# Kernel optimization log

Measured on AMD Instinct MI355X. Metric: run time of the kernel, lower is better.

The kernel has to match this reference:

```python
import jax, jax.numpy as jnp
import numpy as np

B, N, S = 64, 256, 2000
BETA = 0.95
K = int(round(S * (1.0 - BETA)))  # = 100, exact top-k CVaR reformulation
BIL = 4
SAFETY = 0.5
T_DF = 5.0
JITTER = 1e-4  # CHOLESKY_JITTER
N_ITERS = 200


def setup_inputs() -> dict:
    key = jax.random.key(0)
    k1, k2, k3 = jax.random.split(key, 3)
    mu = 0.01 * jax.random.normal(k1, (B, N), dtype=jnp.float32)
    # PSD covariance: sigma = A A^T / N
    A = 0.02 * jax.random.normal(k2, (B, N, N), dtype=jnp.float32)
    sigma = jnp.einsum('bij,bkj->bik', A, A) / N
    # standardized Student-T noise (matches _sample_noise with df>2)
    eps = jax.random.t(k3, T_DF, (B, S, N)) / jnp.sqrt(T_DF / (T_DF - 2.0))
    return {'mu': mu, 'sigma': sigma, 'eps': eps.astype(jnp.float32),
            'is_crisis': 1, 'lambda_risk': 0}


def _simplex_proj(v, z):
    # Euclidean projection of each row of v onto {x >= 0, sum(x) = z}
    n = v.shape[-1]
    u = jnp.flip(jnp.sort(v, axis=-1), axis=-1)          # descending
    css = jnp.cumsum(u, axis=-1) - z
    ind = jnp.arange(1, n + 1, dtype=v.dtype)
    rho = jnp.sum((u - css / ind) > 0, axis=-1)           # (B,) >= 1
    theta = jnp.take_along_axis(css, rho[:, None] - 1, axis=-1) / rho[:, None].astype(v.dtype)
    return jnp.maximum(v - theta, 0.0)


def _solve_cvar(R, floor):
    # minimize CVaR_beta(-R w) = mean of top-K scenario losses,
    # s.t. sum(w)=1, w>=0, w[BIL] >= floor[BIL]  (projected subgradient)
    b, n = R.shape[0], R.shape[2]
    mass = 1.0 - floor.sum()

    def proj(w):
        return _simplex_proj(w - floor, mass) + floor

    w0 = proj(jnp.full((b, n), 1.0 / n, dtype=R.dtype))

    def step(w, t):
        losses = -jnp.einsum('bsn,bn->bs', R, w)          # (B,S)
        thresh = jax.lax.top_k(losses, K)[0][:, -1:]      # K-th largest loss
        m = (losses >= thresh).astype(R.dtype)
        m = m / jnp.maximum(m.sum(-1, keepdims=True), float(K))
        g = -jnp.einsum('bs,bsn->bn', m, R)               # subgradient of top-K mean
        lr = 0.5 / jnp.sqrt(t + 1.0)
        return proj(w - lr * g), None

    w, _ = jax.lax.scan(step, w0, jnp.arange(N_ITERS, dtype=R.dtype))
    return w


def reference(mu, sigma, eps, is_crisis, lambda_risk):
    # 1) Cholesky reparameterization sampling: R = mu + eps @ L^T
    L = jnp.linalg.cholesky(sigma + JITTER * jnp.eye(N, dtype=sigma.dtype))
    R = mu[:, None, :] + jnp.einsum('bsn,bmn->bsm', eps, L)  # (B,S,N)
    if lambda_risk > 0:
        R = R + mu[:, None, :] / max(float(lambda_risk), 0.1)
    # 2) safety floor on BIL when in crisis
    floor = jnp.zeros((N,), dtype=mu.dtype).at[BIL].set(SAFETY * float(is_crisis))
    # 3) batched CVaR solve
    w = _solve_cvar(R, floor)
    # 4) post clamp + renormalize (as in the torch forward)
    w = jnp.maximum(w, 0.0)
    return w / (w.sum(-1, keepdims=True) + 1e-8)
```

## Files before the change

kernel.cpp:

```cpp
#include <hip/hip_runtime.h>
#include <stdint.h>

#define B_   64
#define N_   256
#define S_   2000
#define K_   100
#define BIL_ 4
#define NITER_ 200
#define JITTER_ 1e-4f
#define SAFETY_ 0.5f
#define PART_ 4
#define SCH_  (S_ / PART_)
#define GS_   50

#define OFF_LC16  ((size_t)0)
#define OFF_LR16  (OFF_LC16 + (size_t)B_ * N_ * N_ / 2)
#define OFF_GT    (OFF_LR16 + (size_t)B_ * N_ * N_ / 2)
#define OFF_GR    (OFF_GT + (size_t)B_ * N_ * S_ / 2)
#define OFF_LOSS  (OFF_GR + (size_t)B_ * S_ * N_ / 2)
#define OFF_BAR   (OFF_LOSS + (size_t)2 * B_ * S_)

__device__ __forceinline__ float wred_f(float x) {
#pragma unroll
  for (int off = 32; off > 0; off >>= 1) x += __shfl_xor(x, off);
  return x;
}
__device__ __forceinline__ int wred_i(int x) {
#pragma unroll
  for (int off = 32; off > 0; off >>= 1) x += __shfl_xor(x, off);
  return x;
}
__device__ __forceinline__ unsigned keyd(float x) {
  unsigned u = __float_as_uint(x);
  unsigned ku = (u & 0x80000000u) ? ~u : (u | 0x80000000u);
  return ~ku;
}
__device__ __forceinline__ uint16_t f2b(float f) {
  uint32_t u = __float_as_uint(f);
  uint32_t r = u + 0x7FFFu + ((u >> 16) & 1u);
  return (uint16_t)(r >> 16);
}
__device__ __forceinline__ float blo(uint32_t u) { return __uint_as_float(u << 16); }
__device__ __forceinline__ float bhi(uint32_t u) { return __uint_as_float(u & 0xFFFF0000u); }

__device__ __forceinline__ float michelot4(const float vp[4], float z) {
  bool act[4] = {true, true, true, true};
  float theta = 0.0f;
  int prev = -1;
  for (int pass = 0; pass < 300; ++pass) {
    float ls = 0.0f; int lc = 0;
#pragma unroll
    for (int j = 0; j < 4; ++j) { if (act[j]) { ls += vp[j]; lc += 1; } }
    ls = wred_f(ls);
    lc = wred_i(lc);
    theta = (ls - z) / (float)lc;
    if (lc == prev) break;
    prev = lc;
#pragma unroll
    for (int j = 0; j < 4; ++j) act[j] = (vp[j] > theta);
  }
  return theta;
}

__device__ __forceinline__ void proj_store(const float y[4], float fl_bil, float mass, float muf,
                                           const float* __restrict__ muB, int ln,
                                           float* w_s, float* c_sh) {
  float vp[4];
#pragma unroll
  for (int j = 0; j < 4; ++j) {
    const int n = 4 * ln + j;
    vp[j] = y[j] - ((n == BIL_) ? fl_bil : 0.0f);
  }
  const float theta = michelot4(vp, mass);
  const float4 m4 = *(const float4*)(muB + 4 * ln);
  const float mm[4] = {m4.x, m4.y, m4.z, m4.w};
  float wj[4];
  float cp = 0.0f;
#pragma unroll
  for (int j = 0; j < 4; ++j) {
    const int n = 4 * ln + j;
    wj[j] = fmaxf(vp[j] - theta, 0.0f) + ((n == BIL_) ? fl_bil : 0.0f);
    cp = fmaf(muf * mm[j], wj[j], cp);
  }
  cp = wred_f(cp);
  if (ln == 0) *c_sh = cp;
  *(float4*)(w_s + 4 * ln) = make_float4(wj[0], wj[1], wj[2], wj[3]);
}

__global__ __launch_bounds__(512) void chol_kernel(const float* __restrict__ sigma,
                                                   float* __restrict__ Lc) {
  const int b = blockIdx.x;
  const int tid = threadIdx.x;
  const int i = tid & 255;
  const int half = tid >> 8;
  const float* Sg = sigma + (size_t)b * N_ * N_;
  float* L = Lc + (size_t)b * N_ * N_;
  __shared__ __align__(16) float slab[248 * 8];
  __shared__ __align__(16) float spart[256][8];
  __shared__ __align__(16) float pnl[64];

  for (int j0 = 0; j0 < N_; j0 += 8) {
    for (int x = tid; x < j0 * 8; x += 512) {
      const int k = x >> 3, jj = x & 7;
      slab[x] = L[(size_t)k * N_ + (j0 + jj)];
    }
    float s[8];
    if (half == 0) {
#pragma unroll
      for (int jj = 0; jj < 8; ++jj) {
        float a = Sg[(size_t)(j0 + jj) * N_ + i];
        if (i == j0 + jj) a += JITTER_;
        s[jj] = a;
      }
    } else {
#pragma unroll
      for (int jj = 0; jj < 8; ++jj) s[jj] = 0.0f;
    }
    __syncthreads();

    const int kb = half ? (j0 >> 1) : 0;
    const int ke = half ? j0 : (j0 >> 1);
#pragma unroll 4
    for (int k = kb; k < ke; ++k) {
      const float lk = L[(size_t)k * N_ + i];
      const float4 h0 = *(const float4*)&slab[k * 8];
      const float4 h1 = *(const float4*)&slab[k * 8 + 4];
      s[0] = fmaf(-lk, h0.x, s[0]);
      s[1] = fmaf(-lk, h0.y, s[1]);
      s[2] = fmaf(-lk, h0.z, s[2]);
      s[3] = fmaf(-lk, h0.w, s[3]);
      s[4] = fmaf(-lk, h1.x, s[4]);
      s[5] = fmaf(-lk, h1.y, s[5]);
      s[6] = fmaf(-lk, h1.z, s[6]);
      s[7] = fmaf(-lk, h1.w, s[7]);
    }
    if (half == 1) {
      *(float4*)&spart[i][0] = make_float4(s[0], s[1], s[2], s[3]);
      *(float4*)&spart[i][4] = make_float4(s[4], s[5], s[6], s[7]);
    }
    __syncthreads();

    if (half == 0) {
      const float4 p0 = *(const float4*)&spart[i][0];
      const float4 p1 = *(const float4*)&spart[i][4];
      s[0] += p0.x; s[1] += p0.y; s[2] += p0.z; s[3] += p0.w;
      s[4] += p1.x; s[5] += p1.y; s[6] += p1.z; s[7] += p1.w;
      if ((i >> 3) == (j0 >> 3)) {
        const int base = j0 & 63;
        const int r = i & 7;
        float l[8], di[8];
#pragma unroll
        for (int m = 0; m < 8; ++m) {
          const float smv = __shfl(s[m], base + m);
          const float d = sqrtf(smv);
          const float dinv = 1.0f / d;
          di[m] = dinv;
          float lm;
          if (r == m) lm = d;
          else if (r > m) lm = s[m] * dinv;
          else lm = 0.0f;
          l[m] = lm;
#pragma unroll
          for (int mm = m + 1; mm < 8; ++mm) {
            s[mm] = fmaf(-lm, __shfl(lm, base + mm), s[mm]);
          }
        }
#pragma unroll
        for (int m = 0; m < 8; ++m) pnl[r * 8 + m] = (m < r) ? l[m] : ((m == r) ? di[r] : 0.0f);
#pragma unroll
        for (int m = 0; m < 8; ++m) L[(size_t)(j0 + m) * N_ + i] = l[m];
      }
    }
    __syncthreads();

    if (half == 0 && (i >> 3) != (j0 >> 3)) {
      float l[8];
      if (i > j0) {
#pragma unroll
        for (int m = 0; m < 8; ++m) {
          float sm = s[m];
#pragma unroll
          for (int mm = 0; mm < 8; ++mm) {
            if (mm < m) sm = fmaf(-l[mm], pnl[m * 8 + mm], sm);
          }
          l[m] = sm * pnl[m * 8 + m];
        }
      } else {
#pragma unroll
        for (int m = 0; m < 8; ++m) l[m] = 0.0f;
      }
#pragma unroll
      for (int m = 0; m < 8; ++m) L[(size_t)(j0 + m) * N_ + i] = l[m];
    }
    __syncthreads();
  }
}

__global__ __launch_bounds__(256) void lpack_kernel(const float* __restrict__ Lc,
                                                    uint16_t* __restrict__ Lr16) {
  const int b = blockIdx.x;
  const float* Lp = Lc + (size_t)b * N_ * N_;
  uint16_t* R16 = Lr16 + (size_t)b * N_ * N_;
  __shared__ float tl[32][33];
  const int tx = threadIdx.x & 31;
  const int ty = threadIdx.x >> 5;
  for (int kt = 0; kt < 8; ++kt) {
    for (int it = 0; it < 8; ++it) {
#pragma unroll
      for (int rr = 0; rr < 4; ++rr) {
        const int k = kt * 32 + ty + 8 * rr;
        const int ii = it * 32 + tx;
        tl[ty + 8 * rr][tx] = Lp[(size_t)k * N_ + ii];
      }
      __syncthreads();
#pragma unroll
      for (int rr = 0; rr < 4; ++rr) {
        const int ii = it * 32 + ty + 8 * rr;
        const int k = kt * 32 + tx;
        R16[(size_t)ii * N_ + k] = f2b(tl[tx][ty + 8 * rr]);
      }
      __syncthreads();
    }
  }
}

__global__ __launch_bounds__(256) void g_kernel(const float* __restrict__ eps,
                                                const uint16_t* __restrict__ Lr16,
                                                uint16_t* __restrict__ GT16,
                                                uint16_t* __restrict__ GR16,
                                                int* __restrict__ bar) {
  const int b = blockIdx.x;
  const int s0 = blockIdx.y * GS_;
  const int t = threadIdx.x;
  if (b == 0 && blockIdx.y == 0 && t < 64) bar[t] = 0;
  __shared__ __align__(16) uint16_t esh[GS_][N_];
  const float* E = eps + ((size_t)b * S_ + s0) * N_;
  for (int p = 0; p < GS_; ++p) esh[p][t] = f2b(E[(size_t)p * N_ + t]);
  __syncthreads();

  const uint32_t* Lrow = (const uint32_t*)(Lr16 + (size_t)b * N_ * N_) + (size_t)t * (N_ / 2);
  float acc[GS_];
#pragma unroll
  for (int s = 0; s < GS_; ++s) acc[s] = 0.0f;
  const int jmax = (t >> 1) + 1;
  for (int j = 0; j < jmax; ++j) {
    const uint32_t lu = Lrow[j];
    const float l0 = blo(lu), l1 = bhi(lu);
#pragma unroll
    for (int s = 0; s < GS_; ++s) {
      const uint32_t eu = *(const uint32_t*)&esh[s][2 * j];
      acc[s] = fmaf(l1, bhi(eu), fmaf(l0, blo(eu), acc[s]));
    }
  }
  uint16_t* GRb = GR16 + ((size_t)b * S_ + s0) * N_ + t;
  for (int s = 0; s < GS_; ++s) GRb[(size_t)s * N_] = f2b(acc[s]);
  uint32_t* GTb = (uint32_t*)(GT16 + (size_t)b * N_ * S_ + (size_t)t * S_ + s0);
#pragma unroll
  for (int u = 0; u < GS_ / 2; ++u) {
    const uint32_t pk = (uint32_t)f2b(acc[2 * u]) | ((uint32_t)f2b(acc[2 * u + 1]) << 16);
    GTb[u] = pk;
  }
}

__global__ __launch_bounds__(1024) void solve_kernel(
    const float* __restrict__ mu, const int* __restrict__ pcrisis,
    const int* __restrict__ plam, const uint16_t* __restrict__ GT16,
    const uint16_t* __restrict__ GR16, unsigned* __restrict__ lossbits,
    int* __restrict__ bar, float* __restrict__ out) {
  const int bx = blockIdx.x;
  const int b = bx & (B_ - 1);
  const int part = bx >> 6;
  const int t = threadIdx.x;
  const int ln = t & 63;
  const int s0 = part * SCH_;

  __shared__ __align__(16) float w_s[N_];
  __shared__ __align__(16) float scratch[8][N_];
  __shared__ __align__(16) uint16_t lists[S_];
  __shared__ __align__(16) int hist[4][256];
  __shared__ float c_sh;
  __shared__ int lcnt;
  __shared__ float sum_sh;

  const int crisis = pcrisis[0];
  const int lamv = plam[0];
  const float muf = 1.0f + ((lamv > 0) ? (1.0f / fmaxf((float)lamv, 0.1f)) : 0.0f);
  const float fl_bil = SAFETY_ * (float)crisis;
  const float mass = 1.0f - fl_bil;

  const float* muB = mu + (size_t)b * N_;
  const uint32_t* GTB = (const uint32_t*)(GT16 + (size_t)b * N_ * S_);
  const uint32_t* GRB = (const uint32_t*)(GR16 + (size_t)b * S_ * N_);
  float* sc1 = &scratch[0][0];

  const int q = t >> 8;
  const int idx = t & 255;
  const uint32_t* gcol = GTB + (size_t)(64 * q) * (S_ / 2) + (s0 >> 1) + idx;

  if (t < 64) {
    float y[4];
#pragma unroll
    for (int j = 0; j < 4; ++j) y[j] = 1.0f / (float)N_;
    proj_store(y, fl_bil, mass, muf, muB, ln, w_s, &c_sh);
  }
  __syncthreads();

  for (int it = 0; it < NITER_; ++it) {
    if (idx < SCH_ / 2) {
      float a0 = 0.0f, a1 = 0.0f;
#pragma unroll 8
      for (int j = 0; j < 64; ++j) {
        const uint32_t u = gcol[(size_t)j * (S_ / 2)];
        const float ww = w_s[64 * q + j];
        a0 = fmaf(blo(u), ww, a0);
        a1 = fmaf(bhi(u), ww, a1);
      }
      *(float2*)&sc1[q * SCH_ + 2 * idx] = make_float2(a0, a1);
    }
    __syncthreads();

    unsigned* lgbuf = lossbits + ((it & 1) ? (size_t)B_ * S_ : 0) + (size_t)b * S_;
    if (t < SCH_) {
      const float lv = -(c_sh + ((sc1[t] + sc1[SCH_ + t]) + (sc1[2 * SCH_ + t] + sc1[3 * SCH_ + t])));
      __hip_atomic_store(&lgbuf[s0 + t], keyd(lv), __ATOMIC_RELAXED, __HIP_MEMORY_SCOPE_AGENT);
    } else if (t >= 512) {
      for (int x = t - 512; x < 4 * 256; x += 512) ((int*)hist)[x] = 0;
      if (t == 512) lcnt = 0;
    }
    __syncthreads();

    if (t == 0) {
      __hip_atomic_fetch_add(&bar[b], 1, __ATOMIC_RELAXED, __HIP_MEMORY_SCOPE_AGENT);
      const int target = PART_ * (it + 1);
      while (__hip_atomic_load(&bar[b], __ATOMIC_RELAXED, __HIP_MEMORY_SCOPE_AGENT) < target) {
        __builtin_amdgcn_s_sleep(1);
      }
    }
    __syncthreads();

    uint32_t kx = 0xFFFFFFFFu, ky = 0xFFFFFFFFu;
    if (t < S_ / 2) {
      const unsigned long long two = __hip_atomic_load(
          (const unsigned long long*)(lgbuf + 2 * t), __ATOMIC_RELAXED, __HIP_MEMORY_SCOPE_AGENT);
      kx = (uint32_t)two;
      ky = (uint32_t)(two >> 32);
      atomicAdd(&hist[0][kx >> 24], 1);
      atomicAdd(&hist[0][ky >> 24], 1);
    }
    __syncthreads();

    unsigned pref = 0;
    int r = K_;
#pragma unroll
    for (int pass = 0; pass < 4; ++pass) {
      const int shift = 24 - 8 * pass;
      {
        const int4 c4 = *(const int4*)&hist[pass][4 * ln];
        const int c0 = c4.x, c1 = c4.y, c2 = c4.z, c3 = c4.w;
        const int tot = c0 + c1 + c2 + c3;
        int sc = tot;
#pragma unroll
        for (int off = 1; off < 64; off <<= 1) {
          const int o = __shfl_up(sc, off);
          if (ln >= off) sc += o;
        }
        const int excl = sc - tot;
        const bool has = (excl < r) && (r <= sc);
        const unsigned long long bal = __ballot(has);
        const int lstar = __ffsll(bal) - 1;
        const int bc0 = __shfl(c0, lstar);
        const int bc1 = __shfl(c1, lstar);
        const int bc2 = __shfl(c2, lstar);
        const int bexcl = __shfl(excl, lstar);
        const int rr = r - bexcl;
        int d, rn;
        if (rr <= bc0) { d = 0; rn = rr; }
        else if (rr <= bc0 + bc1) { d = 1; rn = rr - bc0; }
        else if (rr <= bc0 + bc1 + bc2) { d = 2; rn = rr - bc0 - bc1; }
        else { d = 3; rn = rr - bc0 - bc1 - bc2; }
        pref |= (unsigned)(4 * lstar + d) << shift;
        r = rn;
      }
      if (pass < 3) {
        const unsigned msk = 0xFFFFFFFFu << shift;
        const int nshift = shift - 8;
        if (t < S_ / 2) {
          if ((kx & msk) == pref) atomicAdd(&hist[pass + 1][(kx >> nshift) & 255], 1);
          if ((ky & msk) == pref) atomicAdd(&hist[pass + 1][(ky >> nshift) & 255], 1);
        }
      } else {
        if (t < S_ / 2) {
          if (kx <= pref) { const int p = atomicAdd(&lcnt, 1); lists[p] = (uint16_t)(2 * t); }
          if (ky <= pref) { const int p = atomicAdd(&lcnt, 1); lists[p] = (uint16_t)(2 * t + 1); }
        }
      }
      __syncthreads();
    }

    const int cnt = lcnt;
    const float weight = 1.0f / (float)((cnt > K_) ? cnt : K_);

    {
      const int rt = t >> 7;
      const int np = t & 127;
      float a0 = 0.0f, a1 = 0.0f;
      for (int p = rt; p < cnt; p += 8) {
        const uint32_t u = GRB[(size_t)lists[p] * (N_ / 2) + np];
        a0 += blo(u);
        a1 += bhi(u);
      }
      *(float2*)&scratch[rt][2 * np] = make_float2(a0, a1);
    }
    __syncthreads();

    if (t < 64) {
      float4 u4 = make_float4(0.0f, 0.0f, 0.0f, 0.0f);
#pragma unroll
      for (int oct = 0; oct < 8; ++oct) {
        const float4 x = *(const float4*)&scratch[oct][4 * ln];
        u4.x += x.x; u4.y += x.y; u4.z += x.z; u4.w += x.w;
      }
      const float lr = 0.5f / sqrtf((float)it + 1.0f);
      const float4 w4 = *(const float4*)(w_s + 4 * ln);
      const float4 m4 = *(const float4*)(muB + 4 * ln);
      float y[4];
      y[0] = w4.x + lr * (muf * m4.x + u4.x * weight);
      y[1] = w4.y + lr * (muf * m4.y + u4.y * weight);
      y[2] = w4.z + lr * (muf * m4.z + u4.z * weight);
      y[3] = w4.w + lr * (muf * m4.w + u4.w * weight);
      proj_store(y, fl_bil, mass, muf, muB, ln, w_s, &c_sh);
    }
    __syncthreads();
  }

  if (part == 0) {
    if (t < 64) {
      const float4 w4 = *(const float4*)(w_s + 4 * ln);
      const float ssum = wred_f(w4.x + w4.y + w4.z + w4.w);
      if (ln == 0) sum_sh = ssum;
    }
    __syncthreads();
    if (t < N_) out[(size_t)b * N_ + t] = fmaxf(w_s[t], 0.0f) / (sum_sh + 1e-8f);
  }
}

extern "C" void kernel_launch(void* const* d_in, const int* in_sizes, int n_in,
                              void* d_out, int out_size, void* d_ws, size_t ws_size,
                              hipStream_t stream) {
  const float* mu = (const float*)d_in[0];
  const float* sigma = (const float*)d_in[1];
  const float* eps = (const float*)d_in[2];
  const int* crisis = (const int*)d_in[3];
  const int* lam = (const int*)d_in[4];
  float* out = (float*)d_out;
  float* ws = (float*)d_ws;

  uint16_t* Lr16 = (uint16_t*)(ws + OFF_LR16);
  uint16_t* GT16 = (uint16_t*)(ws + OFF_GT);
  uint16_t* GR16 = (uint16_t*)(ws + OFF_GR);
  float* Lc = ws + OFF_GR;
  unsigned* lossbits = (unsigned*)(ws + OFF_LOSS);
  int* bar = (int*)(ws + OFF_BAR);

  chol_kernel<<<dim3(B_), dim3(512), 0, stream>>>(sigma, Lc);
  lpack_kernel<<<dim3(B_), dim3(256), 0, stream>>>(Lc, Lr16);
  g_kernel<<<dim3(B_, S_ / GS_), dim3(256), 0, stream>>>(eps, Lr16, GT16, GR16, bar);

  solve_kernel<<<dim3(PART_ * B_), dim3(1024), 0, stream>>>(
      mu, crisis, lam, GT16, GR16, lossbits, bar, out);
}
```

Baseline: 4.205 ms.

## Reduce loss partials via wave shuffles and overlap local histogram with loss compute

```diff
diff --git a/kernel.cpp b/kernel.cpp
--- a/kernel.cpp
+++ b/kernel.cpp
@@ -12,6 +12,8 @@
 #define PART_ 4
 #define SCH_  (S_ / PART_)
 #define GS_   50
+
+#define HIDX(b) ((((b) & 3) << 6) | ((b) >> 2))
 
 #define OFF_LC16  ((size_t)0)
 #define OFF_LR16  (OFF_LC16 + (size_t)B_ * N_ * N_ / 2)
@@ -291,22 +293,28 @@
   const float* muB = mu + (size_t)b * N_;
   const uint32_t* GTB = (const uint32_t*)(GT16 + (size_t)b * N_ * S_);
   const uint32_t* GRB = (const uint32_t*)(GR16 + (size_t)b * S_ * N_);
-  float* sc1 = &scratch[0][0];
-
-  const int q = t >> 8;
-  const int idx = t & 255;
-  const uint32_t* gcol = GTB + (size_t)(64 * q) * (S_ / 2) + (s0 >> 1) + idx;
+
+  const int pidx = t >> 2;
+  const int q = t & 3;
+  const uint32_t* gcol = GTB + (size_t)(64 * q) * (S_ / 2) + (s0 >> 1) + pidx;
 
   if (t < 64) {
     float y[4];
 #pragma unroll
     for (int j = 0; j < 4; ++j) y[j] = 1.0f / (float)N_;
     proj_store(y, fl_bil, mass, muf, muB, ln, w_s, &c_sh);
+  } else if (t < 576) {
+    ((int*)hist)[t - 64] = 0;
+    ((int*)hist)[t - 64 + 512] = 0;
+    if (t == 64) lcnt = 0;
   }
   __syncthreads();
 
   for (int it = 0; it < NITER_; ++it) {
-    if (idx < SCH_ / 2) {
+    const float cc = c_sh;
+    unsigned* lgbuf = lossbits + ((it & 1) ? (size_t)B_ * S_ : 0) + (size_t)b * S_;
+
+    if (t < 1000) {
       float a0 = 0.0f, a1 = 0.0f;
 #pragma unroll 8
       for (int j = 0; j < 64; ++j) {
@@ -315,17 +323,22 @@
         a0 = fmaf(blo(u), ww, a0);
         a1 = fmaf(bhi(u), ww, a1);
       }
-      *(float2*)&sc1[q * SCH_ + 2 * idx] = make_float2(a0, a1);
-    }
-    __syncthreads();
-
-    unsigned* lgbuf = lossbits + ((it & 1) ? (size_t)B_ * S_ : 0) + (size_t)b * S_;
-    if (t < SCH_) {
-      const float lv = -(c_sh + ((sc1[t] + sc1[SCH_ + t]) + (sc1[2 * SCH_ + t] + sc1[3 * SCH_ + t])));
-      __hip_atomic_store(&lgbuf[s0 + t], keyd(lv), __ATOMIC_RELAXED, __HIP_MEMORY_SCOPE_AGENT);
-    } else if (t >= 512) {
-      for (int x = t - 512; x < 4 * 256; x += 512) ((int*)hist)[x] = 0;
-      if (t == 512) lcnt = 0;
+      a0 += __shfl_xor(a0, 1);
+      a1 += __shfl_xor(a1, 1);
+      a0 += __shfl_xor(a0, 2);
+      a1 += __shfl_xor(a1, 2);
+      const uint32_t k0 = keyd(-(cc + a0));
+      const uint32_t k1 = keyd(-(cc + a1));
+      if (q == 0) {
+        const unsigned long long pk =
+            (unsigned long long)k0 | ((unsigned long long)k1 << 32);
+        __hip_atomic_store((unsigned long long*)(lgbuf + s0 + 2 * pidx), pk,
+                           __ATOMIC_RELAXED, __HIP_MEMORY_SCOPE_AGENT);
+      } else if (q == 1) {
+        atomicAdd(&hist[0][HIDX(k0 >> 24)], 1);
+      } else if (q == 2) {
+        atomicAdd(&hist[0][HIDX(k1 >> 24)], 1);
+      }
     }
     __syncthreads();
 
@@ -344,8 +357,11 @@
           (const unsigned long long*)(lgbuf + 2 * t), __ATOMIC_RELAXED, __HIP_MEMORY_SCOPE_AGENT);
       kx = (uint32_t)two;
       ky = (uint32_t)(two >> 32);
-      atomicAdd(&hist[0][kx >> 24], 1);
-      atomicAdd(&hist[0][ky >> 24], 1);
+      const bool own = (t >= (s0 >> 1)) && (t < (s0 >> 1) + SCH_ / 2);
+      if (!own) {
+        atomicAdd(&hist[0][HIDX(kx >> 24)], 1);
+        atomicAdd(&hist[0][HIDX(ky >> 24)], 1);
+      }
     }
     __syncthreads();
 
@@ -355,8 +371,10 @@
     for (int pass = 0; pass < 4; ++pass) {
       const int shift = 24 - 8 * pass;
       {
-        const int4 c4 = *(const int4*)&hist[pass][4 * ln];
-        const int c0 = c4.x, c1 = c4.y, c2 = c4.z, c3 = c4.w;
+        const int c0 = hist[pass][ln];
+        const int c1 = hist[pass][64 + ln];
+        const int c2 = hist[pass][128 + ln];
+        const int c3 = hist[pass][192 + ln];
         const int tot = c0 + c1 + c2 + c3;
         int sc = tot;
 #pragma unroll
@@ -385,8 +403,8 @@
         const unsigned msk = 0xFFFFFFFFu << shift;
         const int nshift = shift - 8;
         if (t < S_ / 2) {
-          if ((kx & msk) == pref) atomicAdd(&hist[pass + 1][(kx >> nshift) & 255], 1);
-          if ((ky & msk) == pref) atomicAdd(&hist[pass + 1][(ky >> nshift) & 255], 1);
+          if ((kx & msk) == pref) atomicAdd(&hist[pass + 1][HIDX((kx >> nshift) & 255)], 1);
+          if ((ky & msk) == pref) atomicAdd(&hist[pass + 1][HIDX((ky >> nshift) & 255)], 1);
         }
       } else {
         if (t < S_ / 2) {
@@ -429,6 +447,10 @@
       y[2] = w4.z + lr * (muf * m4.z + u4.z * weight);
       y[3] = w4.w + lr * (muf * m4.w + u4.w * weight);
       proj_store(y, fl_bil, mass, muf, muB, ln, w_s, &c_sh);
+    } else if (t < 576) {
+      ((int*)hist)[t - 64] = 0;
+      ((int*)hist)[t - 64 + 512] = 0;
+      if (t == 64) lcnt = 0;
     }
     __syncthreads();
   }
```

Result: slower. 4.516 ms (+7.4%).

## Compute losses from row-major GR and drop transposed GT copy

Applied to the files above, without the earlier changes.

```diff
diff --git a/kernel.cpp b/kernel.cpp
--- a/kernel.cpp
+++ b/kernel.cpp
@@ -226,7 +226,6 @@
 
 __global__ __launch_bounds__(256) void g_kernel(const float* __restrict__ eps,
                                                 const uint16_t* __restrict__ Lr16,
-                                                uint16_t* __restrict__ GT16,
                                                 uint16_t* __restrict__ GR16,
                                                 int* __restrict__ bar) {
   const int b = blockIdx.x;
@@ -254,19 +253,12 @@
   }
   uint16_t* GRb = GR16 + ((size_t)b * S_ + s0) * N_ + t;
   for (int s = 0; s < GS_; ++s) GRb[(size_t)s * N_] = f2b(acc[s]);
-  uint32_t* GTb = (uint32_t*)(GT16 + (size_t)b * N_ * S_ + (size_t)t * S_ + s0);
-#pragma unroll
-  for (int u = 0; u < GS_ / 2; ++u) {
-    const uint32_t pk = (uint32_t)f2b(acc[2 * u]) | ((uint32_t)f2b(acc[2 * u + 1]) << 16);
-    GTb[u] = pk;
-  }
 }
 
 __global__ __launch_bounds__(1024) void solve_kernel(
     const float* __restrict__ mu, const int* __restrict__ pcrisis,
-    const int* __restrict__ plam, const uint16_t* __restrict__ GT16,
-    const uint16_t* __restrict__ GR16, unsigned* __restrict__ lossbits,
-    int* __restrict__ bar, float* __restrict__ out) {
+    const int* __restrict__ plam, const uint16_t* __restrict__ GR16,
+    unsigned* __restrict__ lossbits, int* __restrict__ bar, float* __restrict__ out) {
   const int bx = blockIdx.x;
   const int b = bx & (B_ - 1);
   const int part = bx >> 6;
@@ -289,43 +281,52 @@
   const float mass = 1.0f - fl_bil;
 
   const float* muB = mu + (size_t)b * N_;
-  const uint32_t* GTB = (const uint32_t*)(GT16 + (size_t)b * N_ * S_);
   const uint32_t* GRB = (const uint32_t*)(GR16 + (size_t)b * S_ * N_);
-  float* sc1 = &scratch[0][0];
-
-  const int q = t >> 8;
-  const int idx = t & 255;
-  const uint32_t* gcol = GTB + (size_t)(64 * q) * (S_ / 2) + (s0 >> 1) + idx;
+
+  const int wv = t >> 6;
+  const int oc = (t >> 3) & 7;
+  const int u = t & 7;
 
   if (t < 64) {
     float y[4];
 #pragma unroll
     for (int j = 0; j < 4; ++j) y[j] = 1.0f / (float)N_;
     proj_store(y, fl_bil, mass, muf, muB, ln, w_s, &c_sh);
+  } else if (t < 576) {
+    ((int*)hist)[t - 64] = 0;
+    ((int*)hist)[t - 64 + 512] = 0;
+    if (t == 64) lcnt = 0;
   }
   __syncthreads();
 
   for (int it = 0; it < NITER_; ++it) {
-    if (idx < SCH_ / 2) {
-      float a0 = 0.0f, a1 = 0.0f;
-#pragma unroll 8
-      for (int j = 0; j < 64; ++j) {
-        const uint32_t u = gcol[(size_t)j * (S_ / 2)];
-        const float ww = w_s[64 * q + j];
-        a0 = fmaf(blo(u), ww, a0);
-        a1 = fmaf(bhi(u), ww, a1);
-      }
-      *(float2*)&sc1[q * SCH_ + 2 * idx] = make_float2(a0, a1);
-    }
-    __syncthreads();
-
+    const float cc = c_sh;
     unsigned* lgbuf = lossbits + ((it & 1) ? (size_t)B_ * S_ : 0) + (size_t)b * S_;
-    if (t < SCH_) {
-      const float lv = -(c_sh + ((sc1[t] + sc1[SCH_ + t]) + (sc1[2 * SCH_ + t] + sc1[3 * SCH_ + t])));
-      __hip_atomic_store(&lgbuf[s0 + t], keyd(lv), __ATOMIC_RELAXED, __HIP_MEMORY_SCOPE_AGENT);
-    } else if (t >= 512) {
-      for (int x = t - 512; x < 4 * 256; x += 512) ((int*)hist)[x] = 0;
-      if (t == 512) lcnt = 0;
+
+    {
+      const float* wp = w_s + 2 * u;
+#pragma unroll
+      for (int k = 0; k < 4; ++k) {
+        const int sl = k * 128 + wv * 8 + oc;
+        if (sl < SCH_) {
+          const uint32_t* row = GRB + (size_t)(s0 + sl) * (N_ / 2) + u;
+          float acc = 0.0f;
+#pragma unroll
+          for (int m16 = 0; m16 < 16; ++m16) {
+            const uint32_t g = row[8 * m16];
+            const float2 wv2 = *(const float2*)&wp[16 * m16];
+            acc = fmaf(blo(g), wv2.x, acc);
+            acc = fmaf(bhi(g), wv2.y, acc);
+          }
+          acc += __shfl_xor(acc, 1);
+          acc += __shfl_xor(acc, 2);
+          acc += __shfl_xor(acc, 4);
+          if (u == 0) {
+            __hip_atomic_store(&lgbuf[s0 + sl], keyd(-(cc + acc)), __ATOMIC_RELAXED,
+                               __HIP_MEMORY_SCOPE_AGENT);
+          }
+        }
+      }
     }
     __syncthreads();
 
@@ -405,9 +406,9 @@
       const int np = t & 127;
       float a0 = 0.0f, a1 = 0.0f;
       for (int p = rt; p < cnt; p += 8) {
-        const uint32_t u = GRB[(size_t)lists[p] * (N_ / 2) + np];
-        a0 += blo(u);
-        a1 += bhi(u);
+        const uint32_t uu = GRB[(size_t)lists[p] * (N_ / 2) + np];
+        a0 += blo(uu);
+        a1 += bhi(uu);
       }
       *(float2*)&scratch[rt][2 * np] = make_float2(a0, a1);
     }
@@ -429,6 +430,10 @@
       y[2] = w4.z + lr * (muf * m4.z + u4.z * weight);
       y[3] = w4.w + lr * (muf * m4.w + u4.w * weight);
       proj_store(y, fl_bil, mass, muf, muB, ln, w_s, &c_sh);
+    } else if (t < 576) {
+      ((int*)hist)[t - 64] = 0;
+      ((int*)hist)[t - 64 + 512] = 0;
+      if (t == 64) lcnt = 0;
     }
     __syncthreads();
   }
@@ -456,7 +461,6 @@
   float* ws = (float*)d_ws;
 
   uint16_t* Lr16 = (uint16_t*)(ws + OFF_LR16);
-  uint16_t* GT16 = (uint16_t*)(ws + OFF_GT);
   uint16_t* GR16 = (uint16_t*)(ws + OFF_GR);
   float* Lc = ws + OFF_GR;
   unsigned* lossbits = (unsigned*)(ws + OFF_LOSS);
@@ -464,8 +468,8 @@
 
   chol_kernel<<<dim3(B_), dim3(512), 0, stream>>>(sigma, Lc);
   lpack_kernel<<<dim3(B_), dim3(256), 0, stream>>>(Lc, Lr16);
-  g_kernel<<<dim3(B_, S_ / GS_), dim3(256), 0, stream>>>(eps, Lr16, GT16, GR16, bar);
+  g_kernel<<<dim3(B_, S_ / GS_), dim3(256), 0, stream>>>(eps, Lr16, GR16, bar);
 
   solve_kernel<<<dim3(PART_ * B_), dim3(1024), 0, stream>>>(
-      mu, crisis, lam, GT16, GR16, lossbits, bar, out);
-}
+      mu, crisis, lam, GR16, lossbits, bar, out);
+}
```

New measurement: 6.219 ms. 47.9% more time.

## Drop L pack kernel, use fp32 L directly, build local histogram before barrier

Applied to the files above, without the earlier changes.

```diff
diff --git a/kernel.cpp b/kernel.cpp
--- a/kernel.cpp
+++ b/kernel.cpp
@@ -13,9 +13,8 @@
 #define SCH_  (S_ / PART_)
 #define GS_   50
 
-#define OFF_LC16  ((size_t)0)
-#define OFF_LR16  (OFF_LC16 + (size_t)B_ * N_ * N_ / 2)
-#define OFF_GT    (OFF_LR16 + (size_t)B_ * N_ * N_ / 2)
+#define OFF_LCF   ((size_t)0)
+#define OFF_GT    (OFF_LCF + (size_t)B_ * N_ * N_)
 #define OFF_GR    (OFF_GT + (size_t)B_ * N_ * S_ / 2)
 #define OFF_LOSS  (OFF_GR + (size_t)B_ * S_ * N_ / 2)
 #define OFF_BAR   (OFF_LOSS + (size_t)2 * B_ * S_)
@@ -196,36 +195,8 @@
   }
 }
 
-__global__ __launch_bounds__(256) void lpack_kernel(const float* __restrict__ Lc,
-                                                    uint16_t* __restrict__ Lr16) {
-  const int b = blockIdx.x;
-  const float* Lp = Lc + (size_t)b * N_ * N_;
-  uint16_t* R16 = Lr16 + (size_t)b * N_ * N_;
-  __shared__ float tl[32][33];
-  const int tx = threadIdx.x & 31;
-  const int ty = threadIdx.x >> 5;
-  for (int kt = 0; kt < 8; ++kt) {
-    for (int it = 0; it < 8; ++it) {
-#pragma unroll
-      for (int rr = 0; rr < 4; ++rr) {
-        const int k = kt * 32 + ty + 8 * rr;
-        const int ii = it * 32 + tx;
-        tl[ty + 8 * rr][tx] = Lp[(size_t)k * N_ + ii];
-      }
-      __syncthreads();
-#pragma unroll
-      for (int rr = 0; rr < 4; ++rr) {
-        const int ii = it * 32 + ty + 8 * rr;
-        const int k = kt * 32 + tx;
-        R16[(size_t)ii * N_ + k] = f2b(tl[tx][ty + 8 * rr]);
-      }
-      __syncthreads();
-    }
-  }
-}
-
 __global__ __launch_bounds__(256) void g_kernel(const float* __restrict__ eps,
-                                                const uint16_t* __restrict__ Lr16,
+                                                const float* __restrict__ Lc,
                                                 uint16_t* __restrict__ GT16,
                                                 uint16_t* __restrict__ GR16,
                                                 int* __restrict__ bar) {
@@ -233,23 +204,24 @@
   const int s0 = blockIdx.y * GS_;
   const int t = threadIdx.x;
   if (b == 0 && blockIdx.y == 0 && t < 64) bar[t] = 0;
-  __shared__ __align__(16) uint16_t esh[GS_][N_];
+  __shared__ __align__(16) float esh[GS_][N_];
   const float* E = eps + ((size_t)b * S_ + s0) * N_;
-  for (int p = 0; p < GS_; ++p) esh[p][t] = f2b(E[(size_t)p * N_ + t]);
+  for (int p = 0; p < GS_; ++p) esh[p][t] = E[(size_t)p * N_ + t];
   __syncthreads();
 
-  const uint32_t* Lrow = (const uint32_t*)(Lr16 + (size_t)b * N_ * N_) + (size_t)t * (N_ / 2);
+  const float* Lb = Lc + (size_t)b * N_ * N_;
   float acc[GS_];
 #pragma unroll
   for (int s = 0; s < GS_; ++s) acc[s] = 0.0f;
   const int jmax = (t >> 1) + 1;
   for (int j = 0; j < jmax; ++j) {
-    const uint32_t lu = Lrow[j];
-    const float l0 = blo(lu), l1 = bhi(lu);
+    const int n0 = 2 * j;
+    const float l0 = Lb[(size_t)n0 * N_ + t];
+    const float l1 = Lb[(size_t)(n0 + 1) * N_ + t];
 #pragma unroll
     for (int s = 0; s < GS_; ++s) {
-      const uint32_t eu = *(const uint32_t*)&esh[s][2 * j];
-      acc[s] = fmaf(l1, bhi(eu), fmaf(l0, blo(eu), acc[s]));
+      const float2 e = *(const float2*)&esh[s][n0];
+      acc[s] = fmaf(l1, e.y, fmaf(l0, e.x, acc[s]));
     }
   }
   uint16_t* GRb = GR16 + ((size_t)b * S_ + s0) * N_ + t;
@@ -278,6 +250,7 @@
   __shared__ __align__(16) float scratch[8][N_];
   __shared__ __align__(16) uint16_t lists[S_];
   __shared__ __align__(16) int hist[4][256];
+  __shared__ __align__(16) uint32_t klocal[SCH_];
   __shared__ float c_sh;
   __shared__ int lcnt;
   __shared__ float sum_sh;
@@ -302,6 +275,10 @@
 #pragma unroll
     for (int j = 0; j < 4; ++j) y[j] = 1.0f / (float)N_;
     proj_store(y, fl_bil, mass, muf, muB, ln, w_s, &c_sh);
+  } else if (t < 576) {
+    ((int*)hist)[t - 64] = 0;
+    ((int*)hist)[t - 64 + 512] = 0;
+    if (t == 64) lcnt = 0;
   }
   __syncthreads();
 
@@ -322,10 +299,10 @@
     unsigned* lgbuf = lossbits + ((it & 1) ? (size_t)B_ * S_ : 0) + (size_t)b * S_;
     if (t < SCH_) {
       const float lv = -(c_sh + ((sc1[t] + sc1[SCH_ + t]) + (sc1[2 * SCH_ + t] + sc1[3 * SCH_ + t])));
-      __hip_atomic_store(&lgbuf[s0 + t], keyd(lv), __ATOMIC_RELAXED, __HIP_MEMORY_SCOPE_AGENT);
-    } else if (t >= 512) {
-      for (int x = t - 512; x < 4 * 256; x += 512) ((int*)hist)[x] = 0;
-      if (t == 512) lcnt = 0;
+      const uint32_t k = keyd(lv);
+      __hip_atomic_store(&lgbuf[s0 + t], k, __ATOMIC_RELAXED, __HIP_MEMORY_SCOPE_AGENT);
+      klocal[t] = k;
+      atomicAdd(&hist[0][k >> 24], 1);
     }
     __syncthreads();
 
@@ -340,12 +317,19 @@
 
     uint32_t kx = 0xFFFFFFFFu, ky = 0xFFFFFFFFu;
     if (t < S_ / 2) {
-      const unsigned long long two = __hip_atomic_load(
-          (const unsigned long long*)(lgbuf + 2 * t), __ATOMIC_RELAXED, __HIP_MEMORY_SCOPE_AGENT);
-      kx = (uint32_t)two;
-      ky = (uint32_t)(two >> 32);
-      atomicAdd(&hist[0][kx >> 24], 1);
-      atomicAdd(&hist[0][ky >> 24], 1);
+      const int rel = t - (s0 >> 1);
+      if ((unsigned)rel < (unsigned)(SCH_ / 2)) {
+        kx = klocal[2 * rel];
+        ky = klocal[2 * rel + 1];
+      } else {
+        const unsigned long long two = __hip_atomic_load(
+            (const unsigned long long*)(lgbuf + 2 * t), __ATOMIC_RELAXED,
+            __HIP_MEMORY_SCOPE_AGENT);
+        kx = (uint32_t)two;
+        ky = (uint32_t)(two >> 32);
+        atomicAdd(&hist[0][kx >> 24], 1);
+        atomicAdd(&hist[0][ky >> 24], 1);
+      }
     }
     __syncthreads();
 
@@ -429,6 +413,10 @@
       y[2] = w4.z + lr * (muf * m4.z + u4.z * weight);
       y[3] = w4.w + lr * (muf * m4.w + u4.w * weight);
       proj_store(y, fl_bil, mass, muf, muB, ln, w_s, &c_sh);
+    } else if (t < 576) {
+      ((int*)hist)[t - 64] = 0;
+      ((int*)hist)[t - 64 + 512] = 0;
+      if (t == 64) lcnt = 0;
     }
     __syncthreads();
   }
@@ -455,16 +443,14 @@
   float* out = (float*)d_out;
   float* ws = (float*)d_ws;
 
-  uint16_t* Lr16 = (uint16_t*)(ws + OFF_LR16);
+  float* Lc = ws + OFF_LCF;
   uint16_t* GT16 = (uint16_t*)(ws + OFF_GT);
   uint16_t* GR16 = (uint16_t*)(ws + OFF_GR);
-  float* Lc = ws + OFF_GR;
   unsigned* lossbits = (unsigned*)(ws + OFF_LOSS);
   int* bar = (int*)(ws + OFF_BAR);
 
   chol_kernel<<<dim3(B_), dim3(512), 0, stream>>>(sigma, Lc);
-  lpack_kernel<<<dim3(B_), dim3(256), 0, stream>>>(Lc, Lr16);
-  g_kernel<<<dim3(B_, S_ / GS_), dim3(256), 0, stream>>>(eps, Lr16, GT16, GR16, bar);
+  g_kernel<<<dim3(B_, S_ / GS_), dim3(256), 0, stream>>>(eps, Lc, GT16, GR16, bar);
 
   solve_kernel<<<dim3(PART_ * B_), dim3(1024), 0, stream>>>(
       mu, crisis, lam, GT16, GR16, lossbits, bar, out);
```

After: 4.416 ms. 5.0% more time.
